# Optimization experiments

Measured on AMD Instinct MI355X. Metric: run time of the kernel, lower is better.

## Reference

```python
import jax, jax.numpy as jnp
from jax import lax
import numpy as np

B, S, V, E, H = 256, 20, 10000, 128, 256
CONV_SHAPES = ((16, 3), (16, 3))
IMG = 64
SLOPE = 1.0 / 5.5  # LeakyReLU negative slope


def setup_inputs() -> dict:
    key = jax.random.key(0)
    ks = jax.random.split(key, 12)
    rn = lambda k, shp, s: jax.random.normal(k, shp, jnp.float32) * s
    total = 0
    prev = 3
    for I, K in CONV_SHAPES:
        total += I * prev * K * K + I
        prev = I  # total == 2768
    flat = CONV_SHAPES[-1][0] * IMG * IMG  # 65536
    return {
        "questions": jax.random.randint(ks[0], (B, S), 0, V),
        "images": jax.random.normal(ks[1], (B, 3, IMG, IMG), jnp.float32),
        "emb": rn(ks[2], (V, E), 0.1),
        "w_ih": rn(ks[3], (4 * H, E), 1.0 / np.sqrt(E)),
        "w_hh": rn(ks[4], (4 * H, H), 1.0 / np.sqrt(H)),
        "b_ih": jnp.zeros((4 * H,), jnp.float32),
        "b_hh": jnp.zeros((4 * H,), jnp.float32),
        "hw1": rn(ks[5], (H, 4 * H), 1.0 / np.sqrt(H)),
        "hb1": jnp.zeros((4 * H,), jnp.float32),
        "hw2": rn(ks[6], (4 * H, 16 * H), 1.0 / np.sqrt(4 * H)),
        "hb2": jnp.zeros((16 * H,), jnp.float32),
        "hw3": rn(ks[7], (16 * H, total), 0.02),
        "hb3": jnp.zeros((total,), jnp.float32),
        "lw1": rn(ks[8], (flat, 512), 1.0 / np.sqrt(flat)),
        "lb1": jnp.zeros((512,), jnp.float32),
        "lw2": rn(ks[9], (512, 64), 1.0 / np.sqrt(512)),
        "lb2": jnp.zeros((64,), jnp.float32),
        "lw3": rn(ks[10], (64, 2), 1.0 / np.sqrt(64)),
        "lb3": jnp.zeros((2,), jnp.float32),
    }


def _lstm_final_h(xseq, w_ih, w_hh, b_ih, b_hh):
    # xseq: [S, B, E]; PyTorch gate order i, f, g, o
    b = xseq.shape[1]
    hdim = w_hh.shape[1]
    z = jnp.zeros((b, hdim), xseq.dtype)

    def step(carry, xt):
        h, c = carry
        g = xt @ w_ih.T + h @ w_hh.T + b_ih + b_hh
        i, f, gg, o = jnp.split(g, 4, axis=-1)
        c = jax.nn.sigmoid(f) * c + jax.nn.sigmoid(i) * jnp.tanh(gg)
        h = jax.nn.sigmoid(o) * jnp.tanh(c)
        return (h, c), None

    (h, _), _ = lax.scan(step, (z, z), xseq)
    return h


def _conv_batch(x, w, bias):
    # x: [B, Cin, H, W]; w: [B, Cout, Cin, K, K]; bias: [B, Cout]; padding=1
    def one(xi, wi, bi):
        o = lax.conv_general_dilated(xi[None], wi, (1, 1), ((1, 1), (1, 1)))
        return o[0] + bi[:, None, None]

    return jax.vmap(one)(x, w, bias)


def reference(questions, images, emb, w_ih, w_hh, b_ih, b_hh, hw1, hb1, hw2, hb2,
              hw3, hb3, lw1, lb1, lw2, lb2, lw3, lb3):
    xseq = emb[questions].transpose(1, 0, 2)  # [S, B, E]
    task_codes = _lstm_final_h(xseq, w_ih, w_hh, b_ih, b_hh)  # [B, H]
    lrelu = lambda t: jnp.where(t > 0, t, t * SLOPE)
    hcode = lrelu(task_codes @ hw1 + hb1)
    hcode = lrelu(hcode @ hw2 + hb2)
    all_w = hcode @ hw3 + hb3  # [B, total_output_weights]

    bsz = questions.shape[0]
    x = images
    prev = 3
    off = 0
    for I, K in CONV_SHAPES:
        n = prev * I * K * K
        cw = all_w[:, off:off + n].reshape(bsz, I, prev, K, K)
        cb = all_w[:, off + n:off + n + I]
        off += n + I
        x = _conv_batch(x, cw, cb)
        prev = I

    x = x.reshape(bsz, -1)
    x = jax.nn.relu(x @ lw1 + lb1)
    x = jax.nn.relu(x @ lw2 + lb2)
    return x @ lw3 + lb3
```

## Files before the change

### kernel.cpp

```cpp
#include <hip/hip_runtime.h>
#include <hip/hip_bf16.h>
#include <math.h>

constexpr int kB = 256, kS = 20, kE = 128, kH = 256;
constexpr int kTotalW = 2768;
constexpr float kSlope = 1.0f / 5.5f;

typedef __bf16 bf16x8 __attribute__((ext_vector_type(8)));
typedef float  floatx4 __attribute__((ext_vector_type(4)));

__global__ void zero_f32(float* __restrict__ p, int n) {
    for (int i = blockIdx.x * blockDim.x + threadIdx.x; i < n; i += gridDim.x * blockDim.x)
        p[i] = 0.f;
}

__global__ void cvt_bf16(const float* __restrict__ in, __bf16* __restrict__ out, int n) {
    for (int i = blockIdx.x * blockDim.x + threadIdx.x; i < n; i += gridDim.x * blockDim.x)
        out[i] = (__bf16)in[i];
}

__global__ void wsplit_bf16(const float* __restrict__ w, __bf16* __restrict__ whi,
                            __bf16* __restrict__ wlo, int n) {
    for (int i = blockIdx.x * blockDim.x + threadIdx.x; i < n; i += gridDim.x * blockDim.x) {
        float v = w[i];
        __bf16 hi = (__bf16)v;
        whi[i] = hi;
        wlo[i] = (__bf16)(v - (float)hi);
    }
}

__global__ __launch_bounds__(256) void transpose_cvt(
    const float* __restrict__ W, __bf16* __restrict__ Wt, int K, int N) {
    __shared__ float t[32][33];
    const int k0 = blockIdx.x * 32, n0 = blockIdx.y * 32;
    const int tx = threadIdx.x & 31, ty = threadIdx.x >> 5;
#pragma unroll
    for (int j = 0; j < 32; j += 8) {
        int n = n0 + tx, k = k0 + ty + j;
        t[ty + j][tx] = (n < N) ? W[(size_t)k * N + n] : 0.f;
    }
    __syncthreads();
#pragma unroll
    for (int j = 0; j < 32; j += 8) {
        int n = n0 + ty + j, k = k0 + tx;
        if (n < N) Wt[(size_t)n * K + k] = (__bf16)t[tx][ty + j];
    }
}

__device__ __forceinline__ void gload16(const __bf16* g, __bf16* l) {
    __builtin_amdgcn_global_load_lds(
        (const __attribute__((address_space(1))) void*)g,
        (__attribute__((address_space(3))) void*)l, 16, 0, 0);
}

__global__ __launch_bounds__(256) void mfma128(
    const __bf16* __restrict__ A, const __bf16* __restrict__ Bt,
    float* __restrict__ Cacc, int M, int N, int K, int Kchunk) {
    __shared__ __bf16 As[128 * 64];
    __shared__ __bf16 Bs[128 * 64];
    const int m0 = blockIdx.x * 128, n0 = blockIdx.y * 128;
    const int kbeg = blockIdx.z * Kchunk, kend = kbeg + Kchunk;
    const int tid = threadIdx.x, lane = tid & 63, wave = tid >> 6;
    const int wr = (wave >> 1) * 64, wc = (wave & 1) * 64;
    const int srow = lane >> 3, scol = (lane & 7) * 8;
    const int lrow = lane & 15, lk = (lane >> 4) * 8;
    floatx4 acc[4][4] = {};

    for (int k0 = kbeg; k0 < kend; k0 += 64) {
#pragma unroll
        for (int c = 0; c < 4; ++c) {
            const int ch = wave * 4 + c;
            const int rr = ch * 8 + srow;
            gload16(A + (size_t)(m0 + rr) * K + k0 + scol, &As[ch * 512]);
            int nr = n0 + rr; if (nr > N - 1) nr = N - 1;
            gload16(Bt + (size_t)nr * K + k0 + scol, &Bs[ch * 512]);
        }
        __syncthreads();
#pragma unroll
        for (int ks = 0; ks < 2; ++ks) {
            bf16x8 af[4], bfv[4];
#pragma unroll
            for (int m = 0; m < 4; ++m)
                af[m] = *(const bf16x8*)&As[(wr + m * 16 + lrow) * 64 + ks * 32 + lk];
#pragma unroll
            for (int n = 0; n < 4; ++n)
                bfv[n] = *(const bf16x8*)&Bs[(wc + n * 16 + lrow) * 64 + ks * 32 + lk];
#pragma unroll
            for (int m = 0; m < 4; ++m)
#pragma unroll
                for (int n = 0; n < 4; ++n)
                    acc[m][n] = __builtin_amdgcn_mfma_f32_16x16x32_bf16(
                        af[m], bfv[n], acc[m][n], 0, 0, 0);
        }
        __syncthreads();
    }
    const int col = lane & 15, rq = (lane >> 4) * 4;
#pragma unroll
    for (int m = 0; m < 4; ++m)
#pragma unroll
        for (int n = 0; n < 4; ++n)
#pragma unroll
            for (int r = 0; r < 4; ++r) {
                int gm = m0 + wr + m * 16 + rq + r, gn = n0 + wc + n * 16 + col;
                if (gn < N) atomicAdd(&Cacc[(size_t)gm * N + gn], acc[m][n][r]);
            }
}

__global__ void ep_lrelu_bf16(const float* __restrict__ acc, const float* __restrict__ bias,
                              __bf16* __restrict__ out, int M, int N) {
    int i = blockIdx.x * blockDim.x + threadIdx.x;
    if (i < M * N) {
        float v = acc[i] + bias[i % N];
        out[i] = (__bf16)(v > 0.f ? v : v * kSlope);
    }
}
__global__ void ep_bias_f32(const float* __restrict__ acc, const float* __restrict__ bias,
                            float* __restrict__ out, int M, int N) {
    int i = blockIdx.x * blockDim.x + threadIdx.x;
    if (i < M * N) out[i] = acc[i] + bias[i % N];
}

__global__ __launch_bounds__(256) void xih_mfma(
    const int* __restrict__ questions, const __bf16* __restrict__ embb,
    const __bf16* __restrict__ w_ihb, const float* __restrict__ b_ih,
    const float* __restrict__ b_hh, float* __restrict__ xih) {
    __shared__ __bf16 As[64][72];
    __shared__ __bf16 Bs[64][72];
    __shared__ int qs[64];
    const int m0 = blockIdx.x * 64, n0 = blockIdx.y * 64;
    const int tid = threadIdx.x, lane = tid & 63, wave = tid >> 6;
    if (tid < 64) {
        int m = m0 + tid;
        qs[tid] = questions[(m % kB) * kS + (m / kB)];
    }
    __syncthreads();
    floatx4 acc[4] = {};
    for (int k0 = 0; k0 < kE; k0 += 64) {
        for (int i = tid; i < 512; i += 256) {
            int r = i >> 3, seg = i & 7;
            *(uint4*)(&As[r][seg * 8]) =
                *(const uint4*)(embb + (size_t)qs[r] * kE + k0 + seg * 8);
        }
        for (int i = tid; i < 512; i += 256) {
            int r = i >> 3, seg = i & 7;
            *(uint4*)(&Bs[r][seg * 8]) =
                *(const uint4*)(w_ihb + (size_t)(n0 + r) * kE + k0 + seg * 8);
        }
        __syncthreads();
#pragma unroll
        for (int ks = 0; ks < 2; ++ks) {
            bf16x8 af = *(const bf16x8*)(&As[wave * 16 + (lane & 15)][ks * 32 + (lane >> 4) * 8]);
#pragma unroll
            for (int nb = 0; nb < 4; ++nb) {
                bf16x8 bfr = *(const bf16x8*)(&Bs[nb * 16 + (lane & 15)][ks * 32 + (lane >> 4) * 8]);
                acc[nb] = __builtin_amdgcn_mfma_f32_16x16x32_bf16(af, bfr, acc[nb], 0, 0, 0);
            }
        }
        __syncthreads();
    }
    const int col = lane & 15, rq = (lane >> 4) * 4;
#pragma unroll
    for (int nb = 0; nb < 4; ++nb)
#pragma unroll
        for (int r = 0; r < 4; ++r) {
            int m = m0 + wave * 16 + rq + r, n = n0 + nb * 16 + col;
            xih[(size_t)m * 1024 + n] = acc[nb][r] + b_ih[n] + b_hh[n];
        }
}

__global__ __launch_bounds__(256) void lstm_step_mfma(
    const float* __restrict__ xih_t,
    const __bf16* __restrict__ whi,
    const __bf16* __restrict__ wlo,
    const __bf16* __restrict__ hhi_p, const __bf16* __restrict__ hlo_p,
    float* __restrict__ c,
    __bf16* __restrict__ hhi_n, __bf16* __restrict__ hlo_n,
    int first) {
    __shared__ __bf16 Ah[64 * 64];
    __shared__ __bf16 Al[64 * 64];
    __shared__ __bf16 Bh[128 * 64];
    __shared__ __bf16 Bl[128 * 64];
    const int m0 = blockIdx.x * 64, j0 = blockIdx.y * 32;
    const int tid = threadIdx.x, lane = tid & 63, wv = tid >> 6;
    const int srow = lane >> 3, scol = (lane & 7) * 8;
    const int lrow = lane & 15, lk = (lane >> 4) * 8;
    const int col = lane & 15, rq = (lane >> 4) * 4;

    floatx4 acc[8];
#pragma unroll
    for (int nf = 0; nf < 8; ++nf) {
        int g = nf >> 1, jt = nf & 1;
        int n = g * 256 + j0 + jt * 16 + col;
#pragma unroll
        for (int r = 0; r < 4; ++r)
            acc[nf][r] = xih_t[(size_t)(m0 + wv * 16 + rq + r) * 1024 + n];
    }
    if (!first) {
        for (int k0 = 0; k0 < kH; k0 += 64) {
#pragma unroll
            for (int cc = 0; cc < 2; ++cc) {
                int ch = wv * 2 + cc, r = ch * 8 + srow;
                gload16(hhi_p + (size_t)(m0 + r) * kH + k0 + scol, &Ah[ch * 512]);
                gload16(hlo_p + (size_t)(m0 + r) * kH + k0 + scol, &Al[ch * 512]);
            }
#pragma unroll
            for (int cc = 0; cc < 4; ++cc) {
                int ch = wv * 4 + cc, bn = ch * 8 + srow;
                size_t wrow = (size_t)((bn >> 5) * 256 + j0 + (bn & 31));
                gload16(whi + wrow * kH + k0 + scol, &Bh[ch * 512]);
                gload16(wlo + wrow * kH + k0 + scol, &Bl[ch * 512]);
            }
            __syncthreads();
#pragma unroll
            for (int ks = 0; ks < 2; ++ks) {
                bf16x8 ah = *(const bf16x8*)&Ah[(wv * 16 + lrow) * 64 + ks * 32 + lk];
                bf16x8 al = *(const bf16x8*)&Al[(wv * 16 + lrow) * 64 + ks * 32 + lk];
#pragma unroll
                for (int nf = 0; nf < 8; ++nf) {
                    bf16x8 bh = *(const bf16x8*)&Bh[(nf * 16 + lrow) * 64 + ks * 32 + lk];
                    bf16x8 bl = *(const bf16x8*)&Bl[(nf * 16 + lrow) * 64 + ks * 32 + lk];
                    acc[nf] = __builtin_amdgcn_mfma_f32_16x16x32_bf16(ah, bh, acc[nf], 0, 0, 0);
                    acc[nf] = __builtin_amdgcn_mfma_f32_16x16x32_bf16(al, bh, acc[nf], 0, 0, 0);
                    acc[nf] = __builtin_amdgcn_mfma_f32_16x16x32_bf16(ah, bl, acc[nf], 0, 0, 0);
                }
            }
            __syncthreads();
        }
    }
#pragma unroll
    for (int jt = 0; jt < 2; ++jt)
#pragma unroll
        for (int r = 0; r < 4; ++r) {
            int b = m0 + wv * 16 + rq + r, j = j0 + jt * 16 + col;
            float gi = acc[0 * 2 + jt][r], gf = acc[1 * 2 + jt][r];
            float gg = acc[2 * 2 + jt][r], go = acc[3 * 2 + jt][r];
            float i_ = 1.f / (1.f + expf(-gi));
            float f_ = 1.f / (1.f + expf(-gf));
            float g_ = tanhf(gg);
            float o_ = 1.f / (1.f + expf(-go));
            float cp = first ? 0.f : c[(size_t)b * kH + j];
            float cn = f_ * cp + i_ * g_;
            c[(size_t)b * kH + j] = cn;
            float h = o_ * tanhf(cn);
            __bf16 hi = (__bf16)h;
            hhi_n[(size_t)b * kH + j] = hi;
            hlo_n[(size_t)b * kH + j] = (__bf16)(h - (float)hi);
        }
}

__global__ void bias_relu(const float* __restrict__ acc, const float* __restrict__ bias,
                          float* __restrict__ out, int M, int N) {
    int i = blockIdx.x * blockDim.x + threadIdx.x;
    if (i < M * N) {
        int n = i % N;
        out[i] = fmaxf(acc[i] + bias[n], 0.f);
    }
}

constexpr int ICH = 16;
constexpr int MCH = 16;

__global__ __launch_bounds__(256) void conv_fused_mfma(
    const float* __restrict__ img,
    const float* __restrict__ all_w,
    __bf16* __restrict__ out) {
    const int b = blockIdx.y;
    const int y0 = blockIdx.x * 8;
    __shared__ __align__(16) __bf16 w1a[5 * 16 * 32];
    __shared__ __align__(16) __bf16 w2a[5 * 16 * 32];
    __shared__ float bias_s[32];
    __shared__ __align__(16) __bf16 img_s[12 * 66 * ICH];
    __shared__ __align__(16) __bf16 mid_s[10 * 66 * MCH];

    const int tid = threadIdx.x, lane = tid & 63, wave = tid >> 6;
    const float* wb = all_w + (size_t)b * kTotalW;

    for (int i = tid; i < 12 * 66 * ICH / 8; i += 256)
        ((uint4*)img_s)[i] = make_uint4(0u, 0u, 0u, 0u);
    for (int i = tid; i < 10 * 66 * MCH / 8; i += 256)
        ((uint4*)mid_s)[i] = make_uint4(0u, 0u, 0u, 0u);
    for (int i = tid; i < 2560; i += 256) {
        int p = i >> 9, rem = i & 511, o = rem >> 5, k = rem & 31;
        int half = k >> 4, c = k & 15, t = 2 * p + half;
        w1a[i] = (__bf16)((c < 3 && t < 9) ? wb[o * 27 + c * 9 + t] : 0.f);
    }
    for (int i = tid; i < 2560; i += 256) {
        int p = i >> 9, rem = i & 511, o = rem >> 5, k = rem & 31;
        int half = k >> 4, c = k & 15, t = 2 * p + half;
        w2a[i] = (__bf16)((t < 9) ? wb[448 + (o * 16 + c) * 9 + t] : 0.f);
    }
    if (tid < 16) bias_s[tid] = wb[432 + tid];
    else if (tid < 32) bias_s[tid] = wb[2752 + (tid - 16)];
    __syncthreads();

    for (int i = tid; i < 3 * 12 * 64; i += 256) {
        int c = i / 768, rem = i - c * 768, r = rem >> 6, x = rem & 63;
        int gy = y0 - 2 + r;
        if (gy >= 0 && gy < 64)
            img_s[(r * 66 + (x + 1)) * ICH + c] =
                (__bf16)img[(((size_t)b * 3 + c) << 12) + (gy << 6) + x];
    }
    __syncthreads();

    const int n = lane & 15, half = lane >> 5;
    const int c0 = ((lane >> 4) & 1) * 8, o0 = (lane >> 4) * 4;
    int dy_[5], dx_[5];
#pragma unroll
    for (int p = 0; p < 5; ++p) {
        int t = 2 * p + half;
        dy_[p] = (t < 9) ? t / 3 : 0;
        dx_[p] = (t < 9) ? t % 3 : 0;
    }
    bf16x8 a1[5], a2[5];
#pragma unroll
    for (int p = 0; p < 5; ++p) {
        a1[p] = *(const bf16x8*)&w1a[p * 512 + n * 32 + (lane >> 4) * 8];
        a2[p] = *(const bf16x8*)&w2a[p * 512 + n * 32 + (lane >> 4) * 8];
    }

#pragma unroll
    for (int ti = 0; ti < 10; ++ti) {
        int tile = wave * 10 + ti;
        int rr = tile >> 2, xt = (tile & 3) * 16;
        int gy = y0 - 1 + rr;
        if (gy >= 0 && gy < 64) {
            floatx4 acc = {};
#pragma unroll
            for (int p = 0; p < 5; ++p) {
                bf16x8 bfr = *(const bf16x8*)
                    &img_s[((rr + dy_[p]) * 66 + (xt + n + dx_[p])) * ICH + c0];
                acc = __builtin_amdgcn_mfma_f32_16x16x32_bf16(a1[p], bfr, acc, 0, 0, 0);
            }
            union { short4 s4; __bf16 h[4]; } u;
#pragma unroll
            for (int q = 0; q < 4; ++q) u.h[q] = (__bf16)(acc[q] + bias_s[o0 + q]);
            *(short4*)&mid_s[(rr * 66 + (xt + n + 1)) * MCH + o0] = u.s4;
        }
    }
    __syncthreads();

#pragma unroll
    for (int ti = 0; ti < 8; ++ti) {
        int tile = wave * 8 + ti;
        int rr = tile >> 2, xt = (tile & 3) * 16;
        floatx4 acc = {};
#pragma unroll
        for (int p = 0; p < 5; ++p) {
            bf16x8 bfr = *(const bf16x8*)
                &mid_s[((rr + dy_[p]) * 66 + (xt + n + dx_[p])) * MCH + c0];
            acc = __builtin_amdgcn_mfma_f32_16x16x32_bf16(a2[p], bfr, acc, 0, 0, 0);
        }
        int gy = y0 + rr, gx = xt + n;
#pragma unroll
        for (int q = 0; q < 4; ++q)
            out[(((size_t)b * 16 + o0 + q) * 64 + gy) * 64 + gx] =
                (__bf16)(acc[q] + bias_s[16 + o0 + q]);
    }
}

__global__ __launch_bounds__(64) void lin23(
    const float* __restrict__ l1out,
    const float* __restrict__ lw2, const float* __restrict__ lb2,
    const float* __restrict__ lw3, const float* __restrict__ lb3,
    float* __restrict__ out) {
    const int b = blockIdx.x, j = threadIdx.x;
    __shared__ float row[512];
    __shared__ float s[64];
    for (int i = j; i < 512; i += 64) row[i] = l1out[(size_t)b * 512 + i];
    __syncthreads();
    float acc = lb2[j];
    for (int k = 0; k < 512; ++k) acc += row[k] * lw2[(size_t)k * 64 + j];
    s[j] = fmaxf(acc, 0.f);
    __syncthreads();
    if (j < 2) {
        float o = lb3[j];
        for (int k = 0; k < 64; ++k) o += s[k] * lw3[(size_t)k * 2 + j];
        out[(size_t)b * 2 + j] = o;
    }
}

extern "C" void kernel_launch(void* const* d_in, const int* in_sizes, int n_in,
                              void* d_out, int out_size, void* d_ws, size_t ws_size,
                              hipStream_t stream) {
    const int* questions = (const int*)d_in[0];
    const float* images  = (const float*)d_in[1];
    const float* emb     = (const float*)d_in[2];
    const float* w_ih    = (const float*)d_in[3];
    const float* w_hh    = (const float*)d_in[4];
    const float* b_ih    = (const float*)d_in[5];
    const float* b_hh    = (const float*)d_in[6];
    const float* hw1     = (const float*)d_in[7];
    const float* hb1     = (const float*)d_in[8];
    const float* hw2     = (const float*)d_in[9];
    const float* hb2     = (const float*)d_in[10];
    const float* hw3     = (const float*)d_in[11];
    const float* hb3     = (const float*)d_in[12];
    const float* lw1     = (const float*)d_in[13];
    const float* lb1     = (const float*)d_in[14];
    const float* lw2     = (const float*)d_in[15];
    const float* lb2     = (const float*)d_in[16];
    const float* lw3     = (const float*)d_in[17];
    const float* lb3     = (const float*)d_in[18];
    float* out = (float*)d_out;

    char* ws = (char*)d_ws;
    size_t off = 0;
    auto alloc = [&](size_t nbytes) -> void* {
        void* p = (void*)(ws + off);
        off += (nbytes + 255) & ~(size_t)255;
        return p;
    };
    float*  big   = (float*)alloc(64ull << 20);
    __bf16* lw1t  = (__bf16*)alloc((size_t)512 * 65536 * 2);
    __bf16* w1t   = (__bf16*)alloc((size_t)1024 * 256 * 2);
    __bf16* w2t   = (__bf16*)alloc((size_t)4096 * 1024 * 2);
    __bf16* embb  = (__bf16*)alloc((size_t)10000 * kE * 2);
    __bf16* w_ihb = (__bf16*)alloc((size_t)1024 * kE * 2);
    __bf16* whib  = (__bf16*)alloc((size_t)1024 * kH * 2);
    __bf16* wlob  = (__bf16*)alloc((size_t)1024 * kH * 2);
    __bf16* hhi0  = (__bf16*)alloc((size_t)kB * kH * 2);
    __bf16* hlo0  = (__bf16*)alloc((size_t)kB * kH * 2);
    __bf16* hhi1  = (__bf16*)alloc((size_t)kB * kH * 2);
    __bf16* hlo1  = (__bf16*)alloc((size_t)kB * kH * 2);
    float*  cbuf  = (float*)alloc((size_t)kB * kH * sizeof(float));
    __bf16* h1b   = (__bf16*)alloc((size_t)kB * 1024 * 2);
    __bf16* h2b   = (__bf16*)alloc((size_t)kB * 4096 * 2);
    float*  accz  = (float*)alloc((size_t)kB * (1024 + 4096 + 2768 + 512) * sizeof(float));
    float*  accA  = accz;
    float*  accB  = accA + (size_t)kB * 1024;
    float*  accC  = accB + (size_t)kB * 4096;
    float*  acc1  = accC + (size_t)kB * 2768;
    float*  allw  = (float*)alloc((size_t)kB * kTotalW * sizeof(float));
    float*  l1out = (float*)alloc((size_t)kB * 512 * sizeof(float));

    float*  xih    = big;
    __bf16* c2out  = (__bf16*)big;
    __bf16* w3t    = (__bf16*)((char*)big + (24ull << 20));
    __bf16* hh[2]  = {hhi0, hhi1};
    __bf16* hl[2]  = {hlo0, hlo1};
    const int nACC = kB * (1024 + 4096 + 2768 + 512);
    zero_f32<<<512, 256, 0, stream>>>(accz, nACC);

    cvt_bf16<<<1280, 256, 0, stream>>>(emb, embb, 10000 * kE);
    cvt_bf16<<<128, 256, 0, stream>>>(w_ih, w_ihb, 1024 * kE);
    wsplit_bf16<<<256, 256, 0, stream>>>(w_hh, whib, wlob, 1024 * kH);
    transpose_cvt<<<dim3(8, 32),   256, 0, stream>>>(hw1, w1t, 256, 1024);
    transpose_cvt<<<dim3(32, 128), 256, 0, stream>>>(hw2, w2t, 1024, 4096);
    transpose_cvt<<<dim3(128, 87), 256, 0, stream>>>(hw3, w3t, 4096, 2768);
    transpose_cvt<<<dim3(2048, 16), 256, 0, stream>>>(lw1, lw1t, 65536, 512);

    xih_mfma<<<dim3(80, 16), 256, 0, stream>>>(questions, embb, w_ihb, b_ih, b_hh, xih);

    for (int t = 0; t < kS; ++t) {
        lstm_step_mfma<<<dim3(4, 8), 256, 0, stream>>>(
            xih + (size_t)t * kB * 1024, whib, wlob,
            hh[t & 1], hl[t & 1], cbuf, hh[(t + 1) & 1], hl[(t + 1) & 1], t == 0);
    }
    __bf16* h0b = hh[0];

    mfma128<<<dim3(2, 8, 4),  256, 0, stream>>>(h0b, w1t, accA, 256, 1024, 256, 64);
    ep_lrelu_bf16<<<1024, 256, 0, stream>>>(accA, hb1, h1b, 256, 1024);
    mfma128<<<dim3(2, 32, 4), 256, 0, stream>>>(h1b, w2t, accB, 256, 4096, 1024, 256);
    ep_lrelu_bf16<<<4096, 256, 0, stream>>>(accB, hb2, h2b, 256, 4096);
    mfma128<<<dim3(2, 22, 8), 256, 0, stream>>>(h2b, w3t, accC, 256, 2768, 4096, 512);
    ep_bias_f32<<<2768, 256, 0, stream>>>(accC, hb3, allw, 256, 2768);

    conv_fused_mfma<<<dim3(8, 256), 256, 0, stream>>>(images, allw, c2out);

    mfma128<<<dim3(2, 4, 64), 256, 0, stream>>>(c2out, lw1t, acc1, 256, 512, 65536, 1024);
    bias_relu<<<512, 256, 0, stream>>>(acc1, lb1, l1out, 256, 512);

    lin23<<<256, 64, 0, stream>>>(l1out, lw2, lb2, lw3, lb3, out);
}
```

Measured before the change: 767.6 us.

## Fuse LSTM time steps into one persistent kernel with LDS-resident weights

```diff
diff --git a/kernel.cpp b/kernel.cpp
--- a/kernel.cpp
+++ b/kernel.cpp
@@ -168,84 +168,108 @@
         }
 }
 
-__global__ __launch_bounds__(256) void lstm_step_mfma(
-    const float* __restrict__ xih_t,
+__global__ __launch_bounds__(256, 1) void lstm_persist(
+    const float* __restrict__ xih,
     const __bf16* __restrict__ whi,
     const __bf16* __restrict__ wlo,
-    const __bf16* __restrict__ hhi_p, const __bf16* __restrict__ hlo_p,
-    float* __restrict__ c,
-    __bf16* __restrict__ hhi_n, __bf16* __restrict__ hlo_n,
-    int first) {
+    __bf16* __restrict__ hhi0, __bf16* __restrict__ hlo0,
+    __bf16* __restrict__ hhi1, __bf16* __restrict__ hlo1,
+    int* __restrict__ bar) {
+    __shared__ __bf16 Wh[128 * 256];
+    __shared__ __bf16 Wl[128 * 256];
     __shared__ __bf16 Ah[64 * 64];
     __shared__ __bf16 Al[64 * 64];
-    __shared__ __bf16 Bh[128 * 64];
-    __shared__ __bf16 Bl[128 * 64];
-    const int m0 = blockIdx.x * 64, j0 = blockIdx.y * 32;
+    const int mb = blockIdx.x, m0 = mb * 64, j0 = blockIdx.y * 32;
     const int tid = threadIdx.x, lane = tid & 63, wv = tid >> 6;
     const int srow = lane >> 3, scol = (lane & 7) * 8;
     const int lrow = lane & 15, lk = (lane >> 4) * 8;
     const int col = lane & 15, rq = (lane >> 4) * 4;
 
-    floatx4 acc[8];
-#pragma unroll
-    for (int nf = 0; nf < 8; ++nf) {
-        int g = nf >> 1, jt = nf & 1;
-        int n = g * 256 + j0 + jt * 16 + col;
-#pragma unroll
-        for (int r = 0; r < 4; ++r)
-            acc[nf][r] = xih_t[(size_t)(m0 + wv * 16 + rq + r) * 1024 + n];
-    }
-    if (!first) {
-        for (int k0 = 0; k0 < kH; k0 += 64) {
-#pragma unroll
-            for (int cc = 0; cc < 2; ++cc) {
-                int ch = wv * 2 + cc, r = ch * 8 + srow;
-                gload16(hhi_p + (size_t)(m0 + r) * kH + k0 + scol, &Ah[ch * 512]);
-                gload16(hlo_p + (size_t)(m0 + r) * kH + k0 + scol, &Al[ch * 512]);
-            }
-#pragma unroll
-            for (int cc = 0; cc < 4; ++cc) {
-                int ch = wv * 4 + cc, bn = ch * 8 + srow;
-                size_t wrow = (size_t)((bn >> 5) * 256 + j0 + (bn & 31));
-                gload16(whi + wrow * kH + k0 + scol, &Bh[ch * 512]);
-                gload16(wlo + wrow * kH + k0 + scol, &Bl[ch * 512]);
-            }
+    for (int i = tid; i < 4096; i += 256) {
+        int lrr = i >> 5, m8 = i & 31;
+        int g = lrr >> 5, jj = lrr & 31;
+        int grow = g * 256 + j0 + jj;
+        int nf = g * 2 + (jj >> 4), lr = jj & 15;
+        int k = m8 * 8, ks4 = k >> 5, hi8 = (k >> 3) & 3;
+        int dst = ((nf * 8 + ks4) * 64 + hi8 * 16 + lr) * 8;
+        *(bf16x8*)&Wh[dst] = *(const bf16x8*)(whi + (size_t)grow * kH + k);
+        *(bf16x8*)&Wl[dst] = *(const bf16x8*)(wlo + (size_t)grow * kH + k);
+    }
+    __syncthreads();
+
+    float c_reg[2][4] = {};
+    for (int t = 0; t < kS; ++t) {
+        floatx4 acc[8];
+        const float* xb = xih + (size_t)t * kB * 1024;
+#pragma unroll
+        for (int nf = 0; nf < 8; ++nf) {
+            int g = nf >> 1, jt = nf & 1;
+            int n = g * 256 + j0 + jt * 16 + col;
+#pragma unroll
+            for (int r = 0; r < 4; ++r)
+                acc[nf][r] = xb[(size_t)(m0 + wv * 16 + rq + r) * 1024 + n];
+        }
+        if (t > 0) {
+            const __bf16* Hh = (t & 1) ? hhi1 : hhi0;
+            const __bf16* Hl = (t & 1) ? hlo1 : hlo0;
+            for (int k0 = 0; k0 < kH; k0 += 64) {
+#pragma unroll
+                for (int cc = 0; cc < 2; ++cc) {
+                    int ch = wv * 2 + cc, r = ch * 8 + srow;
+                    gload16(Hh + (size_t)(m0 + r) * kH + k0 + scol, &Ah[ch * 512]);
+                    gload16(Hl + (size_t)(m0 + r) * kH + k0 + scol, &Al[ch * 512]);
+                }
+                __syncthreads();
+#pragma unroll
+                for (int ks = 0; ks < 2; ++ks) {
+                    int ks4 = (k0 >> 5) + ks;
+                    bf16x8 ah = *(const bf16x8*)&Ah[(wv * 16 + lrow) * 64 + ks * 32 + lk];
+                    bf16x8 al = *(const bf16x8*)&Al[(wv * 16 + lrow) * 64 + ks * 32 + lk];
+#pragma unroll
+                    for (int nf = 0; nf < 8; ++nf) {
+                        bf16x8 bh = *(const bf16x8*)&Wh[((nf * 8 + ks4) * 64 + lane) * 8];
+                        bf16x8 bl = *(const bf16x8*)&Wl[((nf * 8 + ks4) * 64 + lane) * 8];
+                        acc[nf] = __builtin_amdgcn_mfma_f32_16x16x32_bf16(ah, bh, acc[nf], 0, 0, 0);
+                        acc[nf] = __builtin_amdgcn_mfma_f32_16x16x32_bf16(al, bh, acc[nf], 0, 0, 0);
+                        acc[nf] = __builtin_amdgcn_mfma_f32_16x16x32_bf16(ah, bl, acc[nf], 0, 0, 0);
+                    }
+                }
+                __syncthreads();
+            }
+        }
+        __bf16* Hhn = ((t + 1) & 1) ? hhi1 : hhi0;
+        __bf16* Hln = ((t + 1) & 1) ? hlo1 : hlo0;
+#pragma unroll
+        for (int jt = 0; jt < 2; ++jt)
+#pragma unroll
+            for (int r = 0; r < 4; ++r) {
+                int b = m0 + wv * 16 + rq + r, j = j0 + jt * 16 + col;
+                float gi = acc[0 * 2 + jt][r], gf = acc[1 * 2 + jt][r];
+                float gg = acc[2 * 2 + jt][r], go = acc[3 * 2 + jt][r];
+                float i_ = 1.f / (1.f + expf(-gi));
+                float f_ = 1.f / (1.f + expf(-gf));
+                float g_ = tanhf(gg);
+                float o_ = 1.f / (1.f + expf(-go));
+                float cn = f_ * c_reg[jt][r] + i_ * g_;
+                c_reg[jt][r] = cn;
+                float h = o_ * tanhf(cn);
+                __bf16 hi = (__bf16)h;
+                Hhn[(size_t)b * kH + j] = hi;
+                Hln[(size_t)b * kH + j] = (__bf16)(h - (float)hi);
+            }
+        if (t < kS - 1) {
+            __threadfence();
             __syncthreads();
-#pragma unroll
-            for (int ks = 0; ks < 2; ++ks) {
-                bf16x8 ah = *(const bf16x8*)&Ah[(wv * 16 + lrow) * 64 + ks * 32 + lk];
-                bf16x8 al = *(const bf16x8*)&Al[(wv * 16 + lrow) * 64 + ks * 32 + lk];
-#pragma unroll
-                for (int nf = 0; nf < 8; ++nf) {
-                    bf16x8 bh = *(const bf16x8*)&Bh[(nf * 16 + lrow) * 64 + ks * 32 + lk];
-                    bf16x8 bl = *(const bf16x8*)&Bl[(nf * 16 + lrow) * 64 + ks * 32 + lk];
-                    acc[nf] = __builtin_amdgcn_mfma_f32_16x16x32_bf16(ah, bh, acc[nf], 0, 0, 0);
-                    acc[nf] = __builtin_amdgcn_mfma_f32_16x16x32_bf16(al, bh, acc[nf], 0, 0, 0);
-                    acc[nf] = __builtin_amdgcn_mfma_f32_16x16x32_bf16(ah, bl, acc[nf], 0, 0, 0);
-                }
+            if (tid == 0) {
+                __hip_atomic_fetch_add(&bar[mb], 1, __ATOMIC_RELEASE,
+                                       __HIP_MEMORY_SCOPE_AGENT);
+                while (__hip_atomic_load(&bar[mb], __ATOMIC_ACQUIRE,
+                                         __HIP_MEMORY_SCOPE_AGENT) < 8 * (t + 1))
+                    __builtin_amdgcn_s_sleep(2);
             }
             __syncthreads();
         }
     }
-#pragma unroll
-    for (int jt = 0; jt < 2; ++jt)
-#pragma unroll
-        for (int r = 0; r < 4; ++r) {
-            int b = m0 + wv * 16 + rq + r, j = j0 + jt * 16 + col;
-            float gi = acc[0 * 2 + jt][r], gf = acc[1 * 2 + jt][r];
-            float gg = acc[2 * 2 + jt][r], go = acc[3 * 2 + jt][r];
-            float i_ = 1.f / (1.f + expf(-gi));
-            float f_ = 1.f / (1.f + expf(-gf));
-            float g_ = tanhf(gg);
-            float o_ = 1.f / (1.f + expf(-go));
-            float cp = first ? 0.f : c[(size_t)b * kH + j];
-            float cn = f_ * cp + i_ * g_;
-            c[(size_t)b * kH + j] = cn;
-            float h = o_ * tanhf(cn);
-            __bf16 hi = (__bf16)h;
-            hhi_n[(size_t)b * kH + j] = hi;
-            hlo_n[(size_t)b * kH + j] = (__bf16)(h - (float)hi);
-        }
 }
 
 __global__ void bias_relu(const float* __restrict__ acc, const float* __restrict__ bias,
@@ -422,24 +446,22 @@
     __bf16* hlo0  = (__bf16*)alloc((size_t)kB * kH * 2);
     __bf16* hhi1  = (__bf16*)alloc((size_t)kB * kH * 2);
     __bf16* hlo1  = (__bf16*)alloc((size_t)kB * kH * 2);
-    float*  cbuf  = (float*)alloc((size_t)kB * kH * sizeof(float));
     __bf16* h1b   = (__bf16*)alloc((size_t)kB * 1024 * 2);
     __bf16* h2b   = (__bf16*)alloc((size_t)kB * 4096 * 2);
-    float*  accz  = (float*)alloc((size_t)kB * (1024 + 4096 + 2768 + 512) * sizeof(float));
+    const int nACC = kB * (1024 + 4096 + 2768 + 512);
+    float*  accz  = (float*)alloc((size_t)(nACC + 64) * sizeof(float));
     float*  accA  = accz;
     float*  accB  = accA + (size_t)kB * 1024;
     float*  accC  = accB + (size_t)kB * 4096;
     float*  acc1  = accC + (size_t)kB * 2768;
+    int*    bar   = (int*)(accz + nACC);
     float*  allw  = (float*)alloc((size_t)kB * kTotalW * sizeof(float));
     float*  l1out = (float*)alloc((size_t)kB * 512 * sizeof(float));
 
     float*  xih    = big;
     __bf16* c2out  = (__bf16*)big;
     __bf16* w3t    = (__bf16*)((char*)big + (24ull << 20));
-    __bf16* hh[2]  = {hhi0, hhi1};
-    __bf16* hl[2]  = {hlo0, hlo1};
-    const int nACC = kB * (1024 + 4096 + 2768 + 512);
-    zero_f32<<<512, 256, 0, stream>>>(accz, nACC);
+    zero_f32<<<512, 256, 0, stream>>>(accz, nACC + 64);
 
     cvt_bf16<<<1280, 256, 0, stream>>>(emb, embb, 10000 * kE);
     cvt_bf16<<<128, 256, 0, stream>>>(w_ih, w_ihb, 1024 * kE);
@@ -451,12 +473,9 @@
 
     xih_mfma<<<dim3(80, 16), 256, 0, stream>>>(questions, embb, w_ihb, b_ih, b_hh, xih);
 
-    for (int t = 0; t < kS; ++t) {
-        lstm_step_mfma<<<dim3(4, 8), 256, 0, stream>>>(
-            xih + (size_t)t * kB * 1024, whib, wlob,
-            hh[t & 1], hl[t & 1], cbuf, hh[(t + 1) & 1], hl[(t + 1) & 1], t == 0);
-    }
-    __bf16* h0b = hh[0];
+    lstm_persist<<<dim3(4, 8), 256, 0, stream>>>(
+        xih, whib, wlob, hhi0, hlo0, hhi1, hlo1, bar);
+    __bf16* h0b = hhi0;
 
     mfma128<<<dim3(2, 8, 4),  256, 0, stream>>>(h0b, w1t, accA, 256, 1024, 256, 64);
     ep_lrelu_bf16<<<1024, 256, 0, stream>>>(accA, hb1, h1b, 256, 1024);
```

New measurement: 762.6 us. No clear change (-0.7%).
